# Kernel tuning notes

Measured on AMD Instinct MI355X. Metric: run time of the kernel, lower is better.

## Reference

```python
import jax, jax.numpy as jnp
import numpy as np

EPS_RMS = 1e-8
EPS_Q = 1e-5


def rms_norm(x, scale):
    # full RMSNorm (p=-1): rms = ||x||_2 / sqrt(d); y = scale * x / (rms + eps)
    d = x.shape[-1]
    norm = jnp.linalg.norm(x, axis=-1, keepdims=True)
    rms = norm * (d ** -0.5)
    return scale * (x / (rms + EPS_RMS))


def activation_quant(x):
    # per-token int8 abs-max quant
    s = 127.0 / jnp.clip(jnp.max(jnp.abs(x), axis=-1, keepdims=True), EPS_Q, None)
    return jnp.clip(jnp.round(x * s), -128, 127) / s


def weight_quant(w):
    # per-tensor ternary abs-mean quant
    s = 1.0 / jnp.clip(jnp.mean(jnp.abs(w)), EPS_Q, None)
    return jnp.clip(jnp.round(w * s), -1, 1) / s


def bit_linear(x, w, scale):
    x_q = activation_quant(rms_norm(x, scale))  # forward value of STE
    w_q = weight_quant(w)
    return x_q @ w_q.T


def setup_inputs() -> dict:
    key = jax.random.key(0)
    ks = jax.random.split(key, 4)
    B = 65536
    x = jax.random.normal(ks[0], (B, 784), dtype=jnp.float32)
    w1 = jax.random.normal(ks[1], (128, 784), dtype=jnp.float32) * (784 ** -0.5)
    w2 = jax.random.normal(ks[2], (64, 128), dtype=jnp.float32) * (128 ** -0.5)
    w3 = jax.random.normal(ks[3], (10, 64), dtype=jnp.float32) * (64 ** -0.5)
    return {
        'x': x,
        'w1': w1, 'scale1': jnp.ones((784,), jnp.float32),
        'w2': w2, 'scale2': jnp.ones((128,), jnp.float32),
        'w3': w3, 'scale3': jnp.ones((64,), jnp.float32),
    }


def reference(x, w1, scale1, w2, scale2, w3, scale3):
    h = jax.nn.relu(bit_linear(x, w1, scale1))
    h = jax.nn.relu(bit_linear(h, w2, scale2))
    return bit_linear(h, w3, scale3)
```

## Files before the change

### kernel.cpp

```cpp
#include <hip/hip_runtime.h>
#include <stdint.h>


typedef int   ix4 __attribute__((ext_vector_type(4)));
typedef float fx4 __attribute__((ext_vector_type(4)));

#define MFMA_I8(a, b, c) __builtin_amdgcn_mfma_i32_16x16x64_i8((a), (b), (c), 0, 0, 0)

__device__ __forceinline__ void sync_lds() {
  asm volatile("s_waitcnt lgkmcnt(0)" ::: "memory");
  __builtin_amdgcn_s_barrier();
}
__device__ __forceinline__ void wave_lds_fence() {
  asm volatile("s_waitcnt lgkmcnt(0)" ::: "memory");
}

__global__ __launch_bounds__(256) void prep_mean(
    const float* __restrict__ w1, const float* __restrict__ w2,
    const float* __restrict__ w3, double* __restrict__ sums) {
  __shared__ double red[256];
  const int b = blockIdx.x;
  const float* w; int n, nb, bb, which;
  if (b < 240)      { w = w1; n = 128 * 784; nb = 240; bb = b;       which = 0; }
  else if (b < 248) { w = w2; n = 64 * 128;  nb = 8;   bb = b - 240; which = 1; }
  else              { w = w3; n = 10 * 64;   nb = 1;   bb = 0;       which = 2; }
  double s = 0.0;
  for (int i = bb * 256 + (int)threadIdx.x; i < n; i += nb * 256)
    s += (double)fabsf(w[i]);
  red[threadIdx.x] = s;
  __syncthreads();
  for (int off = 128; off > 0; off >>= 1) {
    if ((int)threadIdx.x < off) red[threadIdx.x] += red[threadIdx.x + off];
    __syncthreads();
  }
  if (threadIdx.x == 0) atomicAdd(&sums[which], red[0]);
}

__global__ __launch_bounds__(256) void prep_quant(
    const float* __restrict__ w1, const float* __restrict__ w2,
    const float* __restrict__ w3, const double* __restrict__ sums,
    int8_t* __restrict__ t1, int8_t* __restrict__ t2,
    int8_t* __restrict__ t3p) {
  const int idx = blockIdx.x * 256 + (int)threadIdx.x;
  const float s1 = 1.0f / fmaxf((float)(sums[0] * (1.0 / (128.0 * 784.0))), 1e-5f);
  const float s2 = 1.0f / fmaxf((float)(sums[1] * (1.0 / (64.0 * 128.0))), 1e-5f);
  const float s3 = 1.0f / fmaxf((float)(sums[2] * (1.0 / (10.0 * 64.0))), 1e-5f);
  if (idx < 128 * 832) {
    const int n = idx / 832, k = idx - n * 832;
    float v = 0.f;
    if (k < 784) v = fminf(fmaxf(rintf(w1[n * 784 + k] * s1), -1.f), 1.f);
    t1[idx] = (int8_t)(int)v;
  } else if (idx < 128 * 832 + 64 * 128) {
    const int i = idx - 128 * 832;
    t2[i] = (int8_t)(int)fminf(fmaxf(rintf(w2[i] * s2), -1.f), 1.f);
  } else if (idx < 128 * 832 + 64 * 128 + 16 * 64) {
    const int i = idx - (128 * 832 + 64 * 128);
    const int n = i >> 6, p = i & 63;
    const int ch = (p >> 2) + 16 * (p & 3);
    float v = 0.f;
    if (n < 10) v = fminf(fmaxf(rintf(w3[n * 64 + ch] * s3), -1.f), 1.f);
    t3p[i] = (int8_t)(int)v;
  }
}

__global__ __launch_bounds__(256)
__attribute__((amdgpu_waves_per_eu(4)))
void ffn_l1(
    const float* __restrict__ x,
    const float* __restrict__ sc1, const float* __restrict__ sc2,
    const int8_t* __restrict__ t1, const double* __restrict__ sums,
    int8_t* __restrict__ q2g, float* __restrict__ inv2g) {
  __shared__ int8_t q1[16 * 848];
  __shared__ float  h1[16 * 132];
  __shared__ float  inv1[16];

  const int tid = threadIdx.x;
  const int l   = tid & 63;
  const int wv  = tid >> 6;
  const int g   = l >> 4;
  const int sl  = l & 15;
  const int token = wv * 4 + g;

  const float m1 = fmaxf((float)(sums[0] * (1.0 / (128.0 * 784.0))), 1e-5f);

  if (tid < 192) {
    const int t = tid / 12, c = tid - (tid / 12) * 12;
    *reinterpret_cast<unsigned*>(&q1[t * 848 + 784 + c * 4]) = 0u;
  }

  const float* rowp = x + (size_t)(blockIdx.x * 16 + token) * 784;

  float ss = 0.f, am = 0.f;
#pragma unroll
  for (int c = 0; c < 12; ++c) {
    fx4 v  = *reinterpret_cast<const fx4*>(rowp + (sl + 16 * c) * 4);
    fx4 s4 = *reinterpret_cast<const fx4*>(sc1 + (sl + 16 * c) * 4);
    ss += v[0] * v[0] + v[1] * v[1] + v[2] * v[2] + v[3] * v[3];
    am = fmaxf(am, fmaxf(fmaxf(fabsf(v[0] * s4[0]), fabsf(v[1] * s4[1])),
                         fmaxf(fabsf(v[2] * s4[2]), fabsf(v[3] * s4[3]))));
  }
  if (sl < 4) {
    fx4 v  = *reinterpret_cast<const fx4*>(rowp + (sl + 192) * 4);
    fx4 s4 = *reinterpret_cast<const fx4*>(sc1 + (sl + 192) * 4);
    ss += v[0] * v[0] + v[1] * v[1] + v[2] * v[2] + v[3] * v[3];
    am = fmaxf(am, fmaxf(fmaxf(fabsf(v[0] * s4[0]), fabsf(v[1] * s4[1])),
                         fmaxf(fabsf(v[2] * s4[2]), fabsf(v[3] * s4[3]))));
  }
#pragma unroll
  for (int m = 1; m < 16; m <<= 1) {
    ss += __shfl_xor(ss, m, 64);
    am = fmaxf(am, __shfl_xor(am, m, 64));
  }
  const float denom = sqrtf(ss) * (1.0f / 28.0f) + 1e-8f;
  const float invd  = 1.0f / denom;
  const float cl    = fmaxf(am * invd, 1e-5f);
  const float gq    = (127.0f / cl) * invd;
  if (sl == 0) inv1[token] = cl * (1.0f / 127.0f);

#pragma unroll
  for (int c = 0; c < 12; ++c) {
    fx4 v  = *reinterpret_cast<const fx4*>(rowp + (sl + 16 * c) * 4);
    fx4 s4 = *reinterpret_cast<const fx4*>(sc1 + (sl + 16 * c) * 4);
    int q0  = (int)fminf(fmaxf(rintf(v[0] * s4[0] * gq), -128.f), 127.f);
    int q1i = (int)fminf(fmaxf(rintf(v[1] * s4[1] * gq), -128.f), 127.f);
    int q2i = (int)fminf(fmaxf(rintf(v[2] * s4[2] * gq), -128.f), 127.f);
    int q3i = (int)fminf(fmaxf(rintf(v[3] * s4[3] * gq), -128.f), 127.f);
    unsigned p = (unsigned)(q0 & 255) | ((unsigned)(q1i & 255) << 8) |
                 ((unsigned)(q2i & 255) << 16) | ((unsigned)(q3i & 255) << 24);
    *reinterpret_cast<unsigned*>(&q1[token * 848 + (sl + 16 * c) * 4]) = p;
  }
  if (sl < 4) {
    fx4 v  = *reinterpret_cast<const fx4*>(rowp + (sl + 192) * 4);
    fx4 s4 = *reinterpret_cast<const fx4*>(sc1 + (sl + 192) * 4);
    int q0  = (int)fminf(fmaxf(rintf(v[0] * s4[0] * gq), -128.f), 127.f);
    int q1i = (int)fminf(fmaxf(rintf(v[1] * s4[1] * gq), -128.f), 127.f);
    int q2i = (int)fminf(fmaxf(rintf(v[2] * s4[2] * gq), -128.f), 127.f);
    int q3i = (int)fminf(fmaxf(rintf(v[3] * s4[3] * gq), -128.f), 127.f);
    unsigned p = (unsigned)(q0 & 255) | ((unsigned)(q1i & 255) << 8) |
                 ((unsigned)(q2i & 255) << 16) | ((unsigned)(q3i & 255) << 24);
    *reinterpret_cast<unsigned*>(&q1[token * 848 + (sl + 192) * 4]) = p;
  }

  sync_lds();

  ix4 acc0 = {0, 0, 0, 0}, acc1 = {0, 0, 0, 0};
  {
    const int8_t* b0p = t1 + (wv * 32 + sl) * 832;
    const int8_t* b1p = b0p + 16 * 832;
#pragma unroll 4
    for (int kk = 0; kk < 13; ++kk) {
      const int k0 = kk * 64 + g * 16;
      ix4 a  = *reinterpret_cast<const ix4*>(&q1[sl * 848 + k0]);
      ix4 b0 = *reinterpret_cast<const ix4*>(b0p + k0);
      ix4 b1 = *reinterpret_cast<const ix4*>(b1p + k0);
      acc0 = MFMA_I8(a, b0, acc0);
      acc1 = MFMA_I8(a, b1, acc1);
    }
  }
#pragma unroll
  for (int r = 0; r < 4; ++r) {
    const int tr = g * 4 + r;
    const float s = inv1[tr] * m1;
    h1[tr * 132 + wv * 32 + sl]      = fmaxf((float)acc0[r] * s, 0.f);
    h1[tr * 132 + wv * 32 + 16 + sl] = fmaxf((float)acc1[r] * s, 0.f);
  }
  sync_lds();

  {
    fx4 v0 = *reinterpret_cast<const fx4*>(&h1[token * 132 + sl * 4]);
    fx4 v1 = *reinterpret_cast<const fx4*>(&h1[token * 132 + 64 + sl * 4]);
    fx4 s0 = *reinterpret_cast<const fx4*>(sc2 + sl * 4);
    fx4 s1 = *reinterpret_cast<const fx4*>(sc2 + 64 + sl * 4);
    float ss2 = v0[0]*v0[0] + v0[1]*v0[1] + v0[2]*v0[2] + v0[3]*v0[3]
              + v1[0]*v1[0] + v1[1]*v1[1] + v1[2]*v1[2] + v1[3]*v1[3];
    float am2 = fmaxf(fmaxf(fmaxf(fabsf(v0[0]*s0[0]), fabsf(v0[1]*s0[1])),
                            fmaxf(fabsf(v0[2]*s0[2]), fabsf(v0[3]*s0[3]))),
                      fmaxf(fmaxf(fabsf(v1[0]*s1[0]), fabsf(v1[1]*s1[1])),
                            fmaxf(fabsf(v1[2]*s1[2]), fabsf(v1[3]*s1[3]))));
#pragma unroll
    for (int m = 1; m < 16; m <<= 1) {
      ss2 += __shfl_xor(ss2, m, 64);
      am2 = fmaxf(am2, __shfl_xor(am2, m, 64));
    }
    const float den2 = sqrtf(ss2) * 0.08838834764831845f + 1e-8f;
    const float id2  = 1.0f / den2;
    const float cl2  = fmaxf(am2 * id2, 1e-5f);
    const float gq2  = (127.0f / cl2) * id2;
    const size_t tok = (size_t)blockIdx.x * 16 + token;
    if (sl == 0) inv2g[tok] = cl2 * (1.0f / 127.0f);
    int a0 = (int)fminf(fmaxf(rintf(v0[0]*s0[0]*gq2), -128.f), 127.f);
    int a1 = (int)fminf(fmaxf(rintf(v0[1]*s0[1]*gq2), -128.f), 127.f);
    int a2 = (int)fminf(fmaxf(rintf(v0[2]*s0[2]*gq2), -128.f), 127.f);
    int a3 = (int)fminf(fmaxf(rintf(v0[3]*s0[3]*gq2), -128.f), 127.f);
    int b0 = (int)fminf(fmaxf(rintf(v1[0]*s1[0]*gq2), -128.f), 127.f);
    int b1 = (int)fminf(fmaxf(rintf(v1[1]*s1[1]*gq2), -128.f), 127.f);
    int b2 = (int)fminf(fmaxf(rintf(v1[2]*s1[2]*gq2), -128.f), 127.f);
    int b3 = (int)fminf(fmaxf(rintf(v1[3]*s1[3]*gq2), -128.f), 127.f);
    unsigned pa = (unsigned)(a0 & 255) | ((unsigned)(a1 & 255) << 8) |
                  ((unsigned)(a2 & 255) << 16) | ((unsigned)(a3 & 255) << 24);
    unsigned pb = (unsigned)(b0 & 255) | ((unsigned)(b1 & 255) << 8) |
                  ((unsigned)(b2 & 255) << 16) | ((unsigned)(b3 & 255) << 24);
    *reinterpret_cast<unsigned*>(q2g + tok * 128 + sl * 4)      = pa;
    *reinterpret_cast<unsigned*>(q2g + tok * 128 + 64 + sl * 4) = pb;
  }
}

__global__ __launch_bounds__(256) void ffn_l23(
    const int8_t* __restrict__ q2g, const float* __restrict__ inv2g,
    const float* __restrict__ sc3,
    const int8_t* __restrict__ t2, const int8_t* __restrict__ t3p,
    const double* __restrict__ sums, float* __restrict__ out) {
  __shared__ int8_t wbuf[4][16 * 64];

  const int tid = threadIdx.x;
  const int l   = tid & 63;
  const int wv  = tid >> 6;
  const int g   = l >> 4;
  const int sl  = l & 15;
  const int wtok0 = (blockIdx.x * 4 + wv) * 16;

  const float m2 = fmaxf((float)(sums[1] * (1.0 / (64.0 * 128.0))), 1e-5f);
  const float m3 = fmaxf((float)(sums[2] * (1.0 / (10.0 * 64.0))), 1e-5f);

  ix4 a0 = *reinterpret_cast<const ix4*>(q2g + (size_t)(wtok0 + sl) * 128 + g * 16);
  ix4 a1 = *reinterpret_cast<const ix4*>(q2g + (size_t)(wtok0 + sl) * 128 + 64 + g * 16);
  fx4 i2 = *reinterpret_cast<const fx4*>(inv2g + wtok0 + 4 * g);

  ix4 acc[4];
#pragma unroll
  for (int nt = 0; nt < 4; ++nt) {
    ix4 c = {0, 0, 0, 0};
    const int8_t* bp = t2 + (nt * 16 + sl) * 128;
    c = MFMA_I8(a0, *reinterpret_cast<const ix4*>(bp + g * 16), c);
    c = MFMA_I8(a1, *reinterpret_cast<const ix4*>(bp + 64 + g * 16), c);
    acc[nt] = c;
  }

  float sc3v[4];
#pragma unroll
  for (int nt = 0; nt < 4; ++nt) sc3v[nt] = sc3[nt * 16 + sl];

  float h2v[4][4];
  float ss3[4] = {0.f, 0.f, 0.f, 0.f}, am3[4] = {0.f, 0.f, 0.f, 0.f};
#pragma unroll
  for (int nt = 0; nt < 4; ++nt)
#pragma unroll
    for (int r = 0; r < 4; ++r) {
      float h = fmaxf((float)acc[nt][r] * i2[r] * m2, 0.f);
      h2v[nt][r] = h;
      ss3[r] += h * h;
      am3[r] = fmaxf(am3[r], fabsf(h * sc3v[nt]));
    }
#pragma unroll
  for (int m = 1; m < 16; m <<= 1) {
#pragma unroll
    for (int r = 0; r < 4; ++r) {
      ss3[r] += __shfl_xor(ss3[r], m, 64);
      am3[r] = fmaxf(am3[r], __shfl_xor(am3[r], m, 64));
    }
  }
  float gq3[4], i3[4];
#pragma unroll
  for (int r = 0; r < 4; ++r) {
    const float den3 = sqrtf(ss3[r]) * 0.125f + 1e-8f;
    const float id3  = 1.0f / den3;
    const float cl3  = fmaxf(am3[r] * id3, 1e-5f);
    gq3[r] = (127.0f / cl3) * id3;
    i3[r]  = cl3 * (1.0f / 127.0f) * m3;
  }

#pragma unroll
  for (int r = 0; r < 4; ++r) {
    int c0 = (int)fminf(fmaxf(rintf(h2v[0][r] * sc3v[0] * gq3[r]), -128.f), 127.f);
    int c1 = (int)fminf(fmaxf(rintf(h2v[1][r] * sc3v[1] * gq3[r]), -128.f), 127.f);
    int c2 = (int)fminf(fmaxf(rintf(h2v[2][r] * sc3v[2] * gq3[r]), -128.f), 127.f);
    int c3 = (int)fminf(fmaxf(rintf(h2v[3][r] * sc3v[3] * gq3[r]), -128.f), 127.f);
    unsigned p = (unsigned)(c0 & 255) | ((unsigned)(c1 & 255) << 8) |
                 ((unsigned)(c2 & 255) << 16) | ((unsigned)(c3 & 255) << 24);
    *reinterpret_cast<unsigned*>(&wbuf[wv][(4 * g + r) * 64 + sl * 4]) = p;
  }
  wave_lds_fence();

  ix4 a3 = *reinterpret_cast<const ix4*>(&wbuf[wv][sl * 64 + g * 16]);
  ix4 b3 = *reinterpret_cast<const ix4*>(t3p + sl * 64 + g * 16);
  ix4 acc3 = {0, 0, 0, 0};
  acc3 = MFMA_I8(a3, b3, acc3);

  if (sl < 10) {
#pragma unroll
    for (int r = 0; r < 4; ++r)
      out[(size_t)(wtok0 + 4 * g + r) * 10 + sl] = (float)acc3[r] * i3[r];
  }
}

extern "C" void kernel_launch(void* const* d_in, const int* in_sizes, int n_in,
                              void* d_out, int out_size, void* d_ws, size_t ws_size,
                              hipStream_t stream) {
  const float* x  = (const float*)d_in[0];
  const float* w1 = (const float*)d_in[1];
  const float* s1 = (const float*)d_in[2];
  const float* w2 = (const float*)d_in[3];
  const float* s2 = (const float*)d_in[4];
  const float* w3 = (const float*)d_in[5];
  const float* s3 = (const float*)d_in[6];
  float* out = (float*)d_out;

  char* ws = (char*)d_ws;
  double* sums = (double*)ws;
  int8_t* t1   = (int8_t*)(ws + 1024);
  int8_t* t2   = (int8_t*)(ws + 107520);
  int8_t* t3p  = (int8_t*)(ws + 115712);
  float*  inv2 = (float*)(ws + 116736);
  int8_t* q2   = (int8_t*)(ws + 378880);

  const int B = in_sizes[0] / 784;
  const int numTiles = B / 16;

  hipMemsetAsync(sums, 0, 3 * sizeof(double), stream);
  prep_mean<<<249, 256, 0, stream>>>(w1, w2, w3, sums);
  const int total_q = 128 * 832 + 64 * 128 + 16 * 64;
  prep_quant<<<(total_q + 255) / 256, 256, 0, stream>>>(w1, w2, w3, sums, t1, t2, t3p);
  ffn_l1<<<numTiles, 256, 0, stream>>>(x, s1, s2, t1, sums, q2, inv2);
  ffn_l23<<<B / 64, 256, 0, stream>>>(q2, inv2, s3, t2, t3p, sums, out);
}
```

Baseline: 332.0 us.

## Make layer-1 kernel persistent with a producer wave double-buffering x via async LDS loads

```diff
diff --git a/kernel.cpp b/kernel.cpp
--- a/kernel.cpp
+++ b/kernel.cpp
@@ -11,8 +11,17 @@
   asm volatile("s_waitcnt lgkmcnt(0)" ::: "memory");
   __builtin_amdgcn_s_barrier();
 }
+__device__ __forceinline__ void wait_vm0() {
+  asm volatile("s_waitcnt vmcnt(0)" ::: "memory");
+}
 __device__ __forceinline__ void wave_lds_fence() {
   asm volatile("s_waitcnt lgkmcnt(0)" ::: "memory");
+}
+
+__device__ __forceinline__ void async_ld16(const float* g, float* l) {
+  __builtin_amdgcn_global_load_lds(
+      (const __attribute__((address_space(1))) void*)g,
+      (__attribute__((address_space(3))) void*)l, 16, 0, 0);
 }
 
 __global__ __launch_bounds__(256) void prep_mean(
@@ -63,145 +72,176 @@
   }
 }
 
-__global__ __launch_bounds__(256)
-__attribute__((amdgpu_waves_per_eu(4)))
-void ffn_l1(
+__global__ __launch_bounds__(320) void ffn_l1(
     const float* __restrict__ x,
     const float* __restrict__ sc1, const float* __restrict__ sc2,
     const int8_t* __restrict__ t1, const double* __restrict__ sums,
-    int8_t* __restrict__ q2g, float* __restrict__ inv2g) {
-  __shared__ int8_t q1[16 * 848];
-  __shared__ float  h1[16 * 132];
-  __shared__ float  inv1[16];
+    int8_t* __restrict__ q2g, float* __restrict__ inv2g,
+    int numTiles, int tilesPerBlock) {
+  __shared__ float  xbuf[2][6272];
+  __shared__ int8_t q1[8 * 848];
+  __shared__ float  h1[8 * 132];
+  __shared__ float  inv1[8];
 
   const int tid = threadIdx.x;
+  const int wv  = tid >> 6;
   const int l   = tid & 63;
-  const int wv  = tid >> 6;
   const int g   = l >> 4;
   const int sl  = l & 15;
-  const int token = wv * 4 + g;
+  const bool prod = (wv == 4);
+  const int cwv = wv;
+  const int token = cwv * 4 + g;
 
   const float m1 = fmaxf((float)(sums[0] * (1.0 / (128.0 * 784.0))), 1e-5f);
 
-  if (tid < 192) {
-    const int t = tid / 12, c = tid - (tid / 12) * 12;
-    *reinterpret_cast<unsigned*>(&q1[t * 848 + 784 + c * 4]) = 0u;
-  }
-
-  const float* rowp = x + (size_t)(blockIdx.x * 16 + token) * 784;
-
-  float ss = 0.f, am = 0.f;
-#pragma unroll
-  for (int c = 0; c < 12; ++c) {
-    fx4 v  = *reinterpret_cast<const fx4*>(rowp + (sl + 16 * c) * 4);
-    fx4 s4 = *reinterpret_cast<const fx4*>(sc1 + (sl + 16 * c) * 4);
-    ss += v[0] * v[0] + v[1] * v[1] + v[2] * v[2] + v[3] * v[3];
-    am = fmaxf(am, fmaxf(fmaxf(fabsf(v[0] * s4[0]), fabsf(v[1] * s4[1])),
-                         fmaxf(fabsf(v[2] * s4[2]), fabsf(v[3] * s4[3]))));
-  }
-  if (sl < 4) {
-    fx4 v  = *reinterpret_cast<const fx4*>(rowp + (sl + 192) * 4);
-    fx4 s4 = *reinterpret_cast<const fx4*>(sc1 + (sl + 192) * 4);
-    ss += v[0] * v[0] + v[1] * v[1] + v[2] * v[2] + v[3] * v[3];
-    am = fmaxf(am, fmaxf(fmaxf(fabsf(v[0] * s4[0]), fabsf(v[1] * s4[1])),
-                         fmaxf(fabsf(v[2] * s4[2]), fabsf(v[3] * s4[3]))));
-  }
-#pragma unroll
-  for (int m = 1; m < 16; m <<= 1) {
-    ss += __shfl_xor(ss, m, 64);
-    am = fmaxf(am, __shfl_xor(am, m, 64));
-  }
-  const float denom = sqrtf(ss) * (1.0f / 28.0f) + 1e-8f;
-  const float invd  = 1.0f / denom;
-  const float cl    = fmaxf(am * invd, 1e-5f);
-  const float gq    = (127.0f / cl) * invd;
-  if (sl == 0) inv1[token] = cl * (1.0f / 127.0f);
-
-#pragma unroll
-  for (int c = 0; c < 12; ++c) {
-    fx4 v  = *reinterpret_cast<const fx4*>(rowp + (sl + 16 * c) * 4);
-    fx4 s4 = *reinterpret_cast<const fx4*>(sc1 + (sl + 16 * c) * 4);
-    int q0  = (int)fminf(fmaxf(rintf(v[0] * s4[0] * gq), -128.f), 127.f);
-    int q1i = (int)fminf(fmaxf(rintf(v[1] * s4[1] * gq), -128.f), 127.f);
-    int q2i = (int)fminf(fmaxf(rintf(v[2] * s4[2] * gq), -128.f), 127.f);
-    int q3i = (int)fminf(fmaxf(rintf(v[3] * s4[3] * gq), -128.f), 127.f);
-    unsigned p = (unsigned)(q0 & 255) | ((unsigned)(q1i & 255) << 8) |
-                 ((unsigned)(q2i & 255) << 16) | ((unsigned)(q3i & 255) << 24);
-    *reinterpret_cast<unsigned*>(&q1[token * 848 + (sl + 16 * c) * 4]) = p;
-  }
-  if (sl < 4) {
-    fx4 v  = *reinterpret_cast<const fx4*>(rowp + (sl + 192) * 4);
-    fx4 s4 = *reinterpret_cast<const fx4*>(sc1 + (sl + 192) * 4);
-    int q0  = (int)fminf(fmaxf(rintf(v[0] * s4[0] * gq), -128.f), 127.f);
-    int q1i = (int)fminf(fmaxf(rintf(v[1] * s4[1] * gq), -128.f), 127.f);
-    int q2i = (int)fminf(fmaxf(rintf(v[2] * s4[2] * gq), -128.f), 127.f);
-    int q3i = (int)fminf(fmaxf(rintf(v[3] * s4[3] * gq), -128.f), 127.f);
-    unsigned p = (unsigned)(q0 & 255) | ((unsigned)(q1i & 255) << 8) |
-                 ((unsigned)(q2i & 255) << 16) | ((unsigned)(q3i & 255) << 24);
-    *reinterpret_cast<unsigned*>(&q1[token * 848 + (sl + 192) * 4]) = p;
-  }
-
+  if (tid < 96) {
+    const int r = tid / 12, c = tid - r * 12;
+    *reinterpret_cast<unsigned*>(&q1[r * 848 + 784 + c * 4]) = 0u;
+  }
+
+  const int t0 = blockIdx.x * tilesPerBlock;
+
+  if (prod && t0 < numTiles) {
+    const float* gs = x + (size_t)t0 * 6272;
+#pragma unroll
+    for (int s = 0; s < 24; ++s)
+      async_ld16(gs + s * 256 + l * 4, &xbuf[0][s * 256]);
+    if (l < 32) async_ld16(gs + 6144 + l * 4, &xbuf[0][6144]);
+    wait_vm0();
+  }
   sync_lds();
 
-  ix4 acc0 = {0, 0, 0, 0}, acc1 = {0, 0, 0, 0};
-  {
-    const int8_t* b0p = t1 + (wv * 32 + sl) * 832;
-    const int8_t* b1p = b0p + 16 * 832;
+  for (int it = 0; it < tilesPerBlock; ++it) {
+    const int t = t0 + it;
+    if (t >= numTiles) break;
+    const int b = it & 1;
+
+    if (prod) {
+      if (it + 1 < tilesPerBlock && t + 1 < numTiles) {
+        const float* gs = x + (size_t)(t + 1) * 6272;
+#pragma unroll
+        for (int s = 0; s < 24; ++s)
+          async_ld16(gs + s * 256 + l * 4, &xbuf[b ^ 1][s * 256]);
+        if (l < 32) async_ld16(gs + 6144 + l * 4, &xbuf[b ^ 1][6144]);
+      }
+    } else if (cwv < 2) {
+      const float* row = &xbuf[b][token * 784];
+      float ss = 0.f, am = 0.f;
+#pragma unroll
+      for (int c = 0; c < 12; ++c) {
+        fx4 v  = *reinterpret_cast<const fx4*>(row + (sl + 16 * c) * 4);
+        fx4 s4 = *reinterpret_cast<const fx4*>(sc1 + (sl + 16 * c) * 4);
+        ss += v[0] * v[0] + v[1] * v[1] + v[2] * v[2] + v[3] * v[3];
+        am = fmaxf(am, fmaxf(fmaxf(fabsf(v[0] * s4[0]), fabsf(v[1] * s4[1])),
+                             fmaxf(fabsf(v[2] * s4[2]), fabsf(v[3] * s4[3]))));
+      }
+      if (sl < 4) {
+        fx4 v  = *reinterpret_cast<const fx4*>(row + (sl + 192) * 4);
+        fx4 s4 = *reinterpret_cast<const fx4*>(sc1 + (sl + 192) * 4);
+        ss += v[0] * v[0] + v[1] * v[1] + v[2] * v[2] + v[3] * v[3];
+        am = fmaxf(am, fmaxf(fmaxf(fabsf(v[0] * s4[0]), fabsf(v[1] * s4[1])),
+                             fmaxf(fabsf(v[2] * s4[2]), fabsf(v[3] * s4[3]))));
+      }
+#pragma unroll
+      for (int m = 1; m < 16; m <<= 1) {
+        ss += __shfl_xor(ss, m, 64);
+        am = fmaxf(am, __shfl_xor(am, m, 64));
+      }
+      const float denom = sqrtf(ss) * (1.0f / 28.0f) + 1e-8f;
+      const float invd  = 1.0f / denom;
+      const float cl    = fmaxf(am * invd, 1e-5f);
+      const float gq    = (127.0f / cl) * invd;
+      if (sl == 0) inv1[token] = cl * (1.0f / 127.0f);
+
+#pragma unroll
+      for (int c = 0; c < 12; ++c) {
+        fx4 v  = *reinterpret_cast<const fx4*>(row + (sl + 16 * c) * 4);
+        fx4 s4 = *reinterpret_cast<const fx4*>(sc1 + (sl + 16 * c) * 4);
+        int q0  = (int)fminf(fmaxf(rintf(v[0] * s4[0] * gq), -128.f), 127.f);
+        int q1i = (int)fminf(fmaxf(rintf(v[1] * s4[1] * gq), -128.f), 127.f);
+        int q2i = (int)fminf(fmaxf(rintf(v[2] * s4[2] * gq), -128.f), 127.f);
+        int q3i = (int)fminf(fmaxf(rintf(v[3] * s4[3] * gq), -128.f), 127.f);
+        unsigned p = (unsigned)(q0 & 255) | ((unsigned)(q1i & 255) << 8) |
+                     ((unsigned)(q2i & 255) << 16) | ((unsigned)(q3i & 255) << 24);
+        *reinterpret_cast<unsigned*>(&q1[token * 848 + (sl + 16 * c) * 4]) = p;
+      }
+      if (sl < 4) {
+        fx4 v  = *reinterpret_cast<const fx4*>(row + (sl + 192) * 4);
+        fx4 s4 = *reinterpret_cast<const fx4*>(sc1 + (sl + 192) * 4);
+        int q0  = (int)fminf(fmaxf(rintf(v[0] * s4[0] * gq), -128.f), 127.f);
+        int q1i = (int)fminf(fmaxf(rintf(v[1] * s4[1] * gq), -128.f), 127.f);
+        int q2i = (int)fminf(fmaxf(rintf(v[2] * s4[2] * gq), -128.f), 127.f);
+        int q3i = (int)fminf(fmaxf(rintf(v[3] * s4[3] * gq), -128.f), 127.f);
+        unsigned p = (unsigned)(q0 & 255) | ((unsigned)(q1i & 255) << 8) |
+                     ((unsigned)(q2i & 255) << 16) | ((unsigned)(q3i & 255) << 24);
+        *reinterpret_cast<unsigned*>(&q1[token * 848 + (sl + 192) * 4]) = p;
+      }
+    }
+    sync_lds();
+
+    if (!prod) {
+      ix4 acc0 = {0, 0, 0, 0}, acc1 = {0, 0, 0, 0};
+      const int8_t* arow = &q1[(sl & 7) * 848];
+      const int8_t* b0p  = t1 + (cwv * 32 + sl) * 832;
+      const int8_t* b1p  = b0p + 16 * 832;
 #pragma unroll 4
-    for (int kk = 0; kk < 13; ++kk) {
-      const int k0 = kk * 64 + g * 16;
-      ix4 a  = *reinterpret_cast<const ix4*>(&q1[sl * 848 + k0]);
-      ix4 b0 = *reinterpret_cast<const ix4*>(b0p + k0);
-      ix4 b1 = *reinterpret_cast<const ix4*>(b1p + k0);
-      acc0 = MFMA_I8(a, b0, acc0);
-      acc1 = MFMA_I8(a, b1, acc1);
-    }
-  }
-#pragma unroll
-  for (int r = 0; r < 4; ++r) {
-    const int tr = g * 4 + r;
-    const float s = inv1[tr] * m1;
-    h1[tr * 132 + wv * 32 + sl]      = fmaxf((float)acc0[r] * s, 0.f);
-    h1[tr * 132 + wv * 32 + 16 + sl] = fmaxf((float)acc1[r] * s, 0.f);
-  }
-  sync_lds();
-
-  {
-    fx4 v0 = *reinterpret_cast<const fx4*>(&h1[token * 132 + sl * 4]);
-    fx4 v1 = *reinterpret_cast<const fx4*>(&h1[token * 132 + 64 + sl * 4]);
-    fx4 s0 = *reinterpret_cast<const fx4*>(sc2 + sl * 4);
-    fx4 s1 = *reinterpret_cast<const fx4*>(sc2 + 64 + sl * 4);
-    float ss2 = v0[0]*v0[0] + v0[1]*v0[1] + v0[2]*v0[2] + v0[3]*v0[3]
-              + v1[0]*v1[0] + v1[1]*v1[1] + v1[2]*v1[2] + v1[3]*v1[3];
-    float am2 = fmaxf(fmaxf(fmaxf(fabsf(v0[0]*s0[0]), fabsf(v0[1]*s0[1])),
-                            fmaxf(fabsf(v0[2]*s0[2]), fabsf(v0[3]*s0[3]))),
-                      fmaxf(fmaxf(fabsf(v1[0]*s1[0]), fabsf(v1[1]*s1[1])),
-                            fmaxf(fabsf(v1[2]*s1[2]), fabsf(v1[3]*s1[3]))));
-#pragma unroll
-    for (int m = 1; m < 16; m <<= 1) {
-      ss2 += __shfl_xor(ss2, m, 64);
-      am2 = fmaxf(am2, __shfl_xor(am2, m, 64));
-    }
-    const float den2 = sqrtf(ss2) * 0.08838834764831845f + 1e-8f;
-    const float id2  = 1.0f / den2;
-    const float cl2  = fmaxf(am2 * id2, 1e-5f);
-    const float gq2  = (127.0f / cl2) * id2;
-    const size_t tok = (size_t)blockIdx.x * 16 + token;
-    if (sl == 0) inv2g[tok] = cl2 * (1.0f / 127.0f);
-    int a0 = (int)fminf(fmaxf(rintf(v0[0]*s0[0]*gq2), -128.f), 127.f);
-    int a1 = (int)fminf(fmaxf(rintf(v0[1]*s0[1]*gq2), -128.f), 127.f);
-    int a2 = (int)fminf(fmaxf(rintf(v0[2]*s0[2]*gq2), -128.f), 127.f);
-    int a3 = (int)fminf(fmaxf(rintf(v0[3]*s0[3]*gq2), -128.f), 127.f);
-    int b0 = (int)fminf(fmaxf(rintf(v1[0]*s1[0]*gq2), -128.f), 127.f);
-    int b1 = (int)fminf(fmaxf(rintf(v1[1]*s1[1]*gq2), -128.f), 127.f);
-    int b2 = (int)fminf(fmaxf(rintf(v1[2]*s1[2]*gq2), -128.f), 127.f);
-    int b3 = (int)fminf(fmaxf(rintf(v1[3]*s1[3]*gq2), -128.f), 127.f);
-    unsigned pa = (unsigned)(a0 & 255) | ((unsigned)(a1 & 255) << 8) |
-                  ((unsigned)(a2 & 255) << 16) | ((unsigned)(a3 & 255) << 24);
-    unsigned pb = (unsigned)(b0 & 255) | ((unsigned)(b1 & 255) << 8) |
-                  ((unsigned)(b2 & 255) << 16) | ((unsigned)(b3 & 255) << 24);
-    *reinterpret_cast<unsigned*>(q2g + tok * 128 + sl * 4)      = pa;
-    *reinterpret_cast<unsigned*>(q2g + tok * 128 + 64 + sl * 4) = pb;
+      for (int kk = 0; kk < 13; ++kk) {
+        const int k0 = kk * 64 + g * 16;
+        ix4 a = *reinterpret_cast<const ix4*>(arow + k0);
+        acc0 = MFMA_I8(a, *reinterpret_cast<const ix4*>(b0p + k0), acc0);
+        acc1 = MFMA_I8(a, *reinterpret_cast<const ix4*>(b1p + k0), acc1);
+      }
+      if (g < 2) {
+#pragma unroll
+        for (int r = 0; r < 4; ++r) {
+          const int tr = g * 4 + r;
+          const float s = inv1[tr] * m1;
+          h1[tr * 132 + cwv * 32 + sl]      = fmaxf((float)acc0[r] * s, 0.f);
+          h1[tr * 132 + cwv * 32 + 16 + sl] = fmaxf((float)acc1[r] * s, 0.f);
+        }
+      }
+    }
+    sync_lds();
+
+    if (!prod && cwv < 2) {
+      fx4 v0 = *reinterpret_cast<const fx4*>(&h1[token * 132 + sl * 4]);
+      fx4 v1 = *reinterpret_cast<const fx4*>(&h1[token * 132 + 64 + sl * 4]);
+      fx4 s0 = *reinterpret_cast<const fx4*>(sc2 + sl * 4);
+      fx4 s1 = *reinterpret_cast<const fx4*>(sc2 + 64 + sl * 4);
+      float ss2 = v0[0]*v0[0] + v0[1]*v0[1] + v0[2]*v0[2] + v0[3]*v0[3]
+                + v1[0]*v1[0] + v1[1]*v1[1] + v1[2]*v1[2] + v1[3]*v1[3];
+      float am2 = fmaxf(fmaxf(fmaxf(fabsf(v0[0]*s0[0]), fabsf(v0[1]*s0[1])),
+                              fmaxf(fabsf(v0[2]*s0[2]), fabsf(v0[3]*s0[3]))),
+                        fmaxf(fmaxf(fabsf(v1[0]*s1[0]), fabsf(v1[1]*s1[1])),
+                              fmaxf(fabsf(v1[2]*s1[2]), fabsf(v1[3]*s1[3]))));
+#pragma unroll
+      for (int m = 1; m < 16; m <<= 1) {
+        ss2 += __shfl_xor(ss2, m, 64);
+        am2 = fmaxf(am2, __shfl_xor(am2, m, 64));
+      }
+      const float den2 = sqrtf(ss2) * 0.08838834764831845f + 1e-8f;
+      const float id2  = 1.0f / den2;
+      const float cl2  = fmaxf(am2 * id2, 1e-5f);
+      const float gq2  = (127.0f / cl2) * id2;
+      const size_t tok = (size_t)t * 8 + token;
+      if (sl == 0) inv2g[tok] = cl2 * (1.0f / 127.0f);
+      int a0 = (int)fminf(fmaxf(rintf(v0[0]*s0[0]*gq2), -128.f), 127.f);
+      int a1 = (int)fminf(fmaxf(rintf(v0[1]*s0[1]*gq2), -128.f), 127.f);
+      int a2 = (int)fminf(fmaxf(rintf(v0[2]*s0[2]*gq2), -128.f), 127.f);
+      int a3 = (int)fminf(fmaxf(rintf(v0[3]*s0[3]*gq2), -128.f), 127.f);
+      int b0 = (int)fminf(fmaxf(rintf(v1[0]*s1[0]*gq2), -128.f), 127.f);
+      int b1 = (int)fminf(fmaxf(rintf(v1[1]*s1[1]*gq2), -128.f), 127.f);
+      int b2 = (int)fminf(fmaxf(rintf(v1[2]*s1[2]*gq2), -128.f), 127.f);
+      int b3 = (int)fminf(fmaxf(rintf(v1[3]*s1[3]*gq2), -128.f), 127.f);
+      unsigned pa = (unsigned)(a0 & 255) | ((unsigned)(a1 & 255) << 8) |
+                    ((unsigned)(a2 & 255) << 16) | ((unsigned)(a3 & 255) << 24);
+      unsigned pb = (unsigned)(b0 & 255) | ((unsigned)(b1 & 255) << 8) |
+                    ((unsigned)(b2 & 255) << 16) | ((unsigned)(b3 & 255) << 24);
+      *reinterpret_cast<unsigned*>(q2g + tok * 128 + sl * 4)      = pa;
+      *reinterpret_cast<unsigned*>(q2g + tok * 128 + 64 + sl * 4) = pb;
+    }
+    if (prod) wait_vm0();
+    sync_lds();
   }
 }
 
@@ -314,12 +354,14 @@
   int8_t* q2   = (int8_t*)(ws + 378880);
 
   const int B = in_sizes[0] / 784;
-  const int numTiles = B / 16;
+  const int numTiles8 = B / 8;
+  const int grid1 = numTiles8 < 512 ? numTiles8 : 512;
+  const int tpb = (numTiles8 + grid1 - 1) / grid1;
 
   hipMemsetAsync(sums, 0, 3 * sizeof(double), stream);
   prep_mean<<<249, 256, 0, stream>>>(w1, w2, w3, sums);
   const int total_q = 128 * 832 + 64 * 128 + 16 * 64;
   prep_quant<<<(total_q + 255) / 256, 256, 0, stream>>>(w1, w2, w3, sums, t1, t2, t3p);
-  ffn_l1<<<numTiles, 256, 0, stream>>>(x, s1, s2, t1, sums, q2, inv2);
+  ffn_l1<<<grid1, 320, 0, stream>>>(x, s1, s2, t1, sums, q2, inv2, numTiles8, tpb);
   ffn_l23<<<B / 64, 256, 0, stream>>>(q2, inv2, s3, t2, t3p, sums, out);
 }
```

Result: slower. 400.7 us (+20.7%).
